# Kernel tuning notes

Hardware: AMD Instinct MI355X
Metric: run time of the kernel (lower is better)

Reference implementation:

```python
import jax, jax.numpy as jnp
import numpy as np

DIM_IN, DIM_H, NUM_CLASSES, TOPK = 384, 512, 2, 6
SCALE = DIM_H ** (-0.5)
LN_EPS = 1e-5


def setup_inputs() -> dict:
    key = jax.random.key(0)
    ks = jax.random.split(key, 16)
    p = lambda k, shape: jax.random.normal(k, shape, dtype=jnp.float32) * 0.02
    return {
        "feats": jax.random.normal(ks[0], (1, 8192, DIM_IN), dtype=jnp.float32),
        "fc1_w": p(ks[1], (DIM_IN, DIM_H)), "fc1_b": jnp.zeros((DIM_H,), jnp.float32),
        "wh_w": p(ks[2], (DIM_H, DIM_H)), "wh_b": jnp.zeros((DIM_H,), jnp.float32),
        "wt_w": p(ks[3], (DIM_H, DIM_H)), "wt_b": jnp.zeros((DIM_H,), jnp.float32),
        "l1_w": p(ks[4], (DIM_H, DIM_H)), "l1_b": jnp.zeros((DIM_H,), jnp.float32),
        "l2_w": p(ks[5], (DIM_H, DIM_H)), "l2_b": jnp.zeros((DIM_H,), jnp.float32),
        "ln_g": jnp.ones((DIM_H,), jnp.float32), "ln_b": jnp.zeros((DIM_H,), jnp.float32),
        "cls_w": p(ks[6], (DIM_H, NUM_CLASSES)), "cls_b": jnp.zeros((NUM_CLASSES,), jnp.float32),
    }


def _wikg_fwd(feats, fc1_w, fc1_b, wh_w, wh_b, wt_w, wt_b,
              l1_w, l1_b, l2_w, l2_b, ln_g, ln_b, cls_w, cls_b):
    lrelu = lambda v: jax.nn.leaky_relu(v, 0.01)
    x = lrelu(feats @ fc1_w + fc1_b)                      # [B,N,D]
    x = (x + x.mean(axis=1, keepdims=True)) * 0.5
    e_h = x @ wh_w + wh_b                                 # [B,N,D]
    e_t = x @ wt_w + wt_b                                 # [B,N,D]
    attn_logit = jnp.einsum('bnd,bmd->bnm', e_h * SCALE, e_t)  # [B,N,N]
    topk_weight, topk_index = jax.lax.top_k(attn_logit, TOPK)  # [B,N,K]
    # gather neighbor tail embeddings: Nb_h[b,n,k] = e_t[b, topk_index[b,n,k]]
    Nb_h = jax.vmap(lambda et, idx: et[idx])(e_t, topk_index)  # [B,N,K,D]
    topk_prob = jax.nn.softmax(topk_weight, axis=2)            # [B,N,K]
    eh_r = topk_prob[..., None] * Nb_h + (1.0 - topk_prob)[..., None] * e_h[:, :, None, :]
    gate = jnp.tanh(e_h[:, :, None, :] + eh_r)                 # [B,N,K,D]
    ka_weight = jnp.einsum('bnkd,bnkd->bnk', Nb_h, gate)       # [B,N,K]
    ka_prob = jax.nn.softmax(ka_weight, axis=2)
    e_Nh = jnp.einsum('bnk,bnkd->bnd', ka_prob, Nb_h)          # [B,N,D]
    # bi-interaction aggregation
    sum_emb = lrelu((e_h + e_Nh) @ l1_w + l1_b)
    bi_emb = lrelu((e_h * e_Nh) @ l2_w + l2_b)
    emb = sum_emb + bi_emb                                     # [B,N,D]
    # dropout is identity in eval mode; mean readout over nodes (B=1 squeezed)
    h = emb[0].mean(axis=0, keepdims=True)                     # [1,D]
    mu = h.mean(axis=-1, keepdims=True)
    var = ((h - mu) ** 2).mean(axis=-1, keepdims=True)
    h = (h - mu) * jax.lax.rsqrt(var + LN_EPS) * ln_g + ln_b
    return h @ cls_w + cls_b                                   # [1,num_classes]


def reference(feats, fc1_w, fc1_b, wh_w, wh_b, wt_w, wt_b,
              l1_w, l1_b, l2_w, l2_b, ln_g, ln_b, cls_w, cls_b):
    return _wikg_fwd(feats, fc1_w, fc1_b, wh_w, wh_b, wt_w, wt_b,
                     l1_w, l1_b, l2_w, l2_b, ln_g, ln_b, cls_w, cls_b)
```

## Files before the change

### kernel.cpp

```cpp
#include <hip/hip_runtime.h>
#include <math.h>

#define DEV __device__ __forceinline__

using frag_ab = __attribute__((ext_vector_type(8))) short;
using frag_cd = __attribute__((ext_vector_type(4))) float;

static constexpr float SCALE_C = 0.04419417382415922f;

DEV unsigned short f2bf(float f) {
    unsigned u = __float_as_uint(f);
    unsigned r = (u + 0x7FFFu + ((u >> 16) & 1u)) >> 16;
    return (unsigned short)r;
}
DEV float bf2f(unsigned short h) { return __uint_as_float(((unsigned)h) << 16); }

DEV void unpack8(uint4 q, float f[8]) {
    f[0] = bf2f((unsigned short)(q.x & 0xFFFFu)); f[1] = bf2f((unsigned short)(q.x >> 16));
    f[2] = bf2f((unsigned short)(q.y & 0xFFFFu)); f[3] = bf2f((unsigned short)(q.y >> 16));
    f[4] = bf2f((unsigned short)(q.z & 0xFFFFu)); f[5] = bf2f((unsigned short)(q.z >> 16));
    f[6] = bf2f((unsigned short)(q.w & 0xFFFFu)); f[7] = bf2f((unsigned short)(q.w >> 16));
}
DEV uint4 pack8(const float f[8]) {
    uint4 q;
    q.x = (unsigned)f2bf(f[0]) | ((unsigned)f2bf(f[1]) << 16);
    q.y = (unsigned)f2bf(f[2]) | ((unsigned)f2bf(f[3]) << 16);
    q.z = (unsigned)f2bf(f[4]) | ((unsigned)f2bf(f[5]) << 16);
    q.w = (unsigned)f2bf(f[6]) | ((unsigned)f2bf(f[7]) << 16);
    return q;
}

DEV unsigned mono(float f) {
    unsigned u = __float_as_uint(f);
    return u ^ ((unsigned)((int)u >> 31) | 0x80000000u);
}
DEV float unmono(unsigned k) {
    unsigned u = (k & 0x80000000u) ? (k & 0x7FFFFFFFu) : ~k;
    return __uint_as_float(u);
}

DEV void gload_lds16(const void* g, void* l) {
    __builtin_amdgcn_global_load_lds(
        (const __attribute__((address_space(1))) void*)g,
        (__attribute__((address_space(3))) void*)l, 16, 0, 0);
}

__global__ void k_conv_bf16(const float* __restrict__ s, unsigned short* __restrict__ d, int n) {
    int i = (blockIdx.x * 256 + threadIdx.x) * 4;
    if (i + 3 < n) {
        float4 v = *(const float4*)(s + i);
        ushort4 o;
        o.x = f2bf(v.x); o.y = f2bf(v.y); o.z = f2bf(v.z); o.w = f2bf(v.w);
        *(ushort4*)(d + i) = o;
    }
}

__global__ void k_transpose_bf16(const float* __restrict__ s, unsigned short* __restrict__ d, int K, int N) {
    int i = blockIdx.x * 256 + threadIdx.x;
    if (i >= K * N) return;
    int n = i / K, k = i - n * K;
    d[i] = f2bf(s[k * N + n]);
}

DEV void stage_async(const unsigned short* __restrict__ g, int ld, int k0, char* lds, int t) {
    const int sub = t >> 3;
    const int b = (t & 7) << 4;
    const int bs = b ^ ((sub & 7) << 4);
    const char* gb = (const char*)(g + k0) + (size_t)sub * (size_t)(ld * 2) + bs;
    char* lb = lds + ((t >> 6) << 10);
    const size_t rstep = (size_t)32 * (ld * 2);
#pragma unroll
    for (int r = 0; r < 4; ++r)
        gload_lds16(gb + r * rstep, lb + r * 4096);
}

DEV void mfma_tile(const char* As, const char* Bs, int lane, int wr, int wc, frag_cd (&acc)[4][4]) {
#pragma unroll
    for (int ks = 0; ks < 2; ++ks) {
        const int boff = ks * 64 + ((lane >> 4) << 4);
        frag_ab av[4];
#pragma unroll
        for (int f = 0; f < 4; ++f) {
            int ra = wr * 64 + f * 16 + (lane & 15);
            av[f] = *(const frag_ab*)(As + ra * 128 + (boff ^ ((ra & 7) << 4)));
        }
#pragma unroll
        for (int j = 0; j < 4; ++j) {
            int rb = wc * 64 + j * 16 + (lane & 15);
            frag_ab bv = *(const frag_ab*)(Bs + rb * 128 + (boff ^ ((rb & 7) << 4)));
#pragma unroll
            for (int i = 0; i < 4; ++i)
                acc[i][j] = __builtin_amdgcn_mfma_f32_16x16x32_bf16(av[i], bv, acc[i][j], 0, 0, 0);
        }
    }
}

template <int ACT, int EPI>
__global__ __launch_bounds__(256, 2) void k_gemm(
    const unsigned short* __restrict__ A0, const unsigned short* __restrict__ A1,
    const unsigned short* __restrict__ B0, const unsigned short* __restrict__ B1,
    const float* __restrict__ bias0, const float* __restrict__ bias1,
    unsigned short* __restrict__ out0, unsigned short* __restrict__ out1,
    float* __restrict__ colsum, int M, int N, int K) {
    __shared__ __align__(16) char smem[65536];
    __shared__ float colacc[128];
    char* sA0 = smem;
    char* sA1 = smem + 16384;
    char* sB0 = smem + 32768;
    char* sB1 = smem + 49152;
    const int z = blockIdx.z;
    const unsigned short* A = z ? A1 : A0;
    const unsigned short* BT = z ? B1 : B0;
    const float* bias = z ? bias1 : bias0;
    unsigned short* out = z ? out1 : out0;
    const int t = threadIdx.x;
    const int lane = t & 63, wid = t >> 6, wr = wid >> 1, wc = wid & 1;
    const int m0 = blockIdx.x * 128, n0 = blockIdx.y * 128;
    if (EPI >= 1 && t < 128) colacc[t] = 0.f;
    const unsigned short* Ap = A + (size_t)m0 * K;
    const unsigned short* Bp = BT + (size_t)n0 * K;
    frag_cd acc[4][4] = {};
    const int nt = K >> 6;
    stage_async(Ap, K, 0, sA0, t);
    stage_async(Bp, K, 0, sB0, t);
    __syncthreads();
#pragma unroll 1
    for (int tt = 0; tt < nt - 2; tt += 2) {
        stage_async(Ap, K, (tt + 1) * 64, sA1, t);
        stage_async(Bp, K, (tt + 1) * 64, sB1, t);
        mfma_tile(sA0, sB0, lane, wr, wc, acc);
        __syncthreads();
        stage_async(Ap, K, (tt + 2) * 64, sA0, t);
        stage_async(Bp, K, (tt + 2) * 64, sB0, t);
        mfma_tile(sA1, sB1, lane, wr, wc, acc);
        __syncthreads();
    }
    stage_async(Ap, K, (nt - 1) * 64, sA1, t);
    stage_async(Bp, K, (nt - 1) * 64, sB1, t);
    mfma_tile(sA0, sB0, lane, wr, wc, acc);
    __syncthreads();
    mfma_tile(sA1, sB1, lane, wr, wc, acc);
    float bval[4];
#pragma unroll
    for (int j = 0; j < 4; ++j) bval[j] = bias[n0 + wc * 64 + j * 16 + (lane & 15)];
#pragma unroll
    for (int i = 0; i < 4; ++i) {
#pragma unroll
        for (int j = 0; j < 4; ++j) {
            float cs = 0.f;
#pragma unroll
            for (int r = 0; r < 4; ++r) {
                float v = acc[i][j][r] + bval[j];
                if (ACT) v = v > 0.f ? v : 0.01f * v;
                if (EPI != 2) {
                    int row = m0 + wr * 64 + i * 16 + (lane >> 4) * 4 + r;
                    int col = n0 + wc * 64 + j * 16 + (lane & 15);
                    out[(size_t)row * N + col] = f2bf(v);
                }
                cs += v;
            }
            if (EPI >= 1) atomicAdd(&colacc[wc * 64 + j * 16 + (lane & 15)], cs);
        }
    }
    if (EPI >= 1) {
        __syncthreads();
        if (t < 128) atomicAdd(&colsum[n0 + t], colacc[t]);
    }
}

__global__ void k_update_x(unsigned short* __restrict__ xb, const float* __restrict__ colsum) {
    int i = (blockIdx.x * 256 + threadIdx.x) * 8;
    uint4 q = *(const uint4*)(xb + i);
    float f[8]; unpack8(q, f);
    int c0 = i & 511;
#pragma unroll
    for (int j = 0; j < 8; ++j) f[j] = 0.5f * (f[j] + colsum[c0 + j] * (1.f / 8192.f));
    *(uint4*)(xb + i) = pack8(f);
}

DEV void kins(unsigned (&v)[6], unsigned k) {
    unsigned m1 = v[0] < k ? v[0] : k;
    unsigned m2 = v[1] < k ? v[1] : k;
    unsigned m3 = v[2] < k ? v[2] : k;
    unsigned m4 = v[3] < k ? v[3] : k;
    unsigned m5 = v[4] < k ? v[4] : k;
    v[0] = v[0] > k ? v[0] : k;
    v[1] = v[1] > m1 ? v[1] : m1;
    v[2] = v[2] > m2 ? v[2] : m2;
    v[3] = v[3] > m3 ? v[3] : m3;
    v[4] = v[4] > m4 ? v[4] : m4;
    v[5] = v[5] > m5 ? v[5] : m5;
}

__global__ __launch_bounds__(256, 2) void k_attn_topk(
    const unsigned short* __restrict__ ehb, const unsigned short* __restrict__ etb,
    unsigned* __restrict__ pk) {
    __shared__ __align__(16) char smem[65536];
    char* sA0 = smem;
    char* sA1 = smem + 16384;
    char* sB0 = smem + 32768;
    char* sB1 = smem + 49152;
    unsigned* Stile = (unsigned*)smem;
    const int t = threadIdx.x;
    const int lane = t & 63, wid = t >> 6, wr = wid >> 1, wc = wid & 1;
    const int m0 = blockIdx.x * 128;
    const int csplit = blockIdx.y;
    const int srow = t >> 1, hh = t & 1;
    const unsigned short* Ap = ehb + (size_t)m0 * 512;
    unsigned ka[6] = {0, 0, 0, 0, 0, 0};
    unsigned kb[6] = {0, 0, 0, 0, 0, 0};

    for (int ct = 0; ct < 4; ++ct) {
        const int n0 = csplit * 512 + ct * 128;
        const unsigned short* Bp = etb + (size_t)n0 * 512;
        frag_cd acc[4][4] = {};
        __syncthreads();
        stage_async(Ap, 512, 0, sA0, t);
        stage_async(Bp, 512, 0, sB0, t);
        __syncthreads();
#pragma unroll 1
        for (int p = 0; p < 3; ++p) {
            stage_async(Ap, 512, (2 * p + 1) * 64, sA1, t);
            stage_async(Bp, 512, (2 * p + 1) * 64, sB1, t);
            mfma_tile(sA0, sB0, lane, wr, wc, acc);
            __syncthreads();
            stage_async(Ap, 512, (2 * p + 2) * 64, sA0, t);
            stage_async(Bp, 512, (2 * p + 2) * 64, sB0, t);
            mfma_tile(sA1, sB1, lane, wr, wc, acc);
            __syncthreads();
        }
        stage_async(Ap, 512, 7 * 64, sA1, t);
        stage_async(Bp, 512, 7 * 64, sB1, t);
        mfma_tile(sA0, sB0, lane, wr, wc, acc);
        __syncthreads();
        mfma_tile(sA1, sB1, lane, wr, wc, acc);
        __syncthreads();
#pragma unroll
        for (int ch = 0; ch < 2; ++ch) {
            if (wc == ch) {
                const unsigned ckb = 8191u - (unsigned)(n0 + ch * 64 + (lane & 15));
#pragma unroll
                for (int i = 0; i < 4; ++i)
#pragma unroll
                    for (int j = 0; j < 4; ++j)
#pragma unroll
                        for (int r = 0; r < 4; ++r) {
                            int row = wr * 64 + i * 16 + (lane >> 4) * 4 + r;
                            int col = j * 16 + (lane & 15);
                            unsigned key = (mono(acc[i][j][r]) & 0xFFFFE000u) | (ckb - j * 16);
                            Stile[row * 68 + col] = key;
                        }
            }
            __syncthreads();
            const uint4* srowp = (const uint4*)(Stile + srow * 68 + hh * 32);
#pragma unroll
            for (int q = 0; q < 8; ++q) {
                uint4 u = srowp[q];
                kins(ka, u.x); kins(kb, u.y);
                kins(ka, u.z); kins(kb, u.w);
            }
            __syncthreads();
        }
    }
#pragma unroll
    for (int j = 0; j < 6; ++j) kins(ka, kb[j]);
#pragma unroll
    for (int j = 0; j < 6; ++j) {
        unsigned ok = (unsigned)__shfl_xor((int)ka[j], 1, 64);
        if (hh == 0) kins(ka, ok);
    }
    if (hh == 0) {
        size_t o = ((size_t)(m0 + srow) * 16 + csplit) * 6;
#pragma unroll
        for (int j = 0; j < 6; ++j) pk[o + j] = ka[j];
    }
}

__global__ void k_merge_topk(const unsigned* __restrict__ pk,
                             float* __restrict__ tw, int* __restrict__ ti) {
    int r = blockIdx.x * 256 + threadIdx.x;
    if (r >= 8192) return;
    unsigned v[6] = {0, 0, 0, 0, 0, 0};
    for (int s2 = 0; s2 < 16; ++s2) {
        const unsigned* p = pk + ((size_t)r * 16 + s2) * 6;
#pragma unroll
        for (int j = 0; j < 6; ++j) kins(v, p[j]);
    }
#pragma unroll
    for (int j = 0; j < 6; ++j) {
        tw[r * 6 + j] = unmono(v[j] & 0xFFFFE000u) * SCALE_C;
        ti[r * 6 + j] = 8191 - (int)(v[j] & 8191u);
    }
}

__global__ __launch_bounds__(256) void k_agg(
    const unsigned short* __restrict__ ehb, const unsigned short* __restrict__ etb,
    const float* __restrict__ tw, const int* __restrict__ ti,
    unsigned short* __restrict__ sb, unsigned short* __restrict__ pb) {
    const int t = threadIdx.x, lane = t & 63, wid = t >> 6;
    const int node = blockIdx.x * 4 + wid;
    const int d0 = lane * 8;
    float w[6]; int idx[6];
#pragma unroll
    for (int k = 0; k < 6; ++k) { w[k] = tw[node * 6 + k]; idx[k] = ti[node * 6 + k]; }
    float mx = w[0];
#pragma unroll
    for (int k = 1; k < 6; ++k) mx = fmaxf(mx, w[k]);
    float pr[6], s = 0.f;
#pragma unroll
    for (int k = 0; k < 6; ++k) { pr[k] = expf(w[k] - mx); s += pr[k]; }
    float inv = 1.f / s;
#pragma unroll
    for (int k = 0; k < 6; ++k) pr[k] *= inv;

    float eh[8]; unpack8(*(const uint4*)(ehb + (size_t)node * 512 + d0), eh);
    float nb[6][8];
#pragma unroll
    for (int k = 0; k < 6; ++k) unpack8(*(const uint4*)(etb + (size_t)idx[k] * 512 + d0), nb[k]);

    float kw[6] = {};
#pragma unroll
    for (int k = 0; k < 6; ++k) {
        float pk2 = pr[k];
#pragma unroll
        for (int j = 0; j < 8; ++j) {
            float ehr = pk2 * nb[k][j] + (1.f - pk2) * eh[j];
            float g = tanhf(eh[j] + ehr);
            kw[k] += nb[k][j] * g;
        }
    }
#pragma unroll
    for (int k = 0; k < 6; ++k)
#pragma unroll
        for (int o = 1; o < 64; o <<= 1) kw[k] += __shfl_xor(kw[k], o, 64);
    float m2 = kw[0];
#pragma unroll
    for (int k = 1; k < 6; ++k) m2 = fmaxf(m2, kw[k]);
    float kp[6], s2 = 0.f;
#pragma unroll
    for (int k = 0; k < 6; ++k) { kp[k] = expf(kw[k] - m2); s2 += kp[k]; }
    float inv2 = 1.f / s2;
#pragma unroll
    for (int k = 0; k < 6; ++k) kp[k] *= inv2;

    float sv[8], pv[8];
#pragma unroll
    for (int j = 0; j < 8; ++j) {
        float en = 0.f;
#pragma unroll
        for (int k = 0; k < 6; ++k) en += kp[k] * nb[k][j];
        sv[j] = eh[j] + en;
        pv[j] = eh[j] * en;
    }
    *(uint4*)(sb + (size_t)node * 512 + d0) = pack8(sv);
    *(uint4*)(pb + (size_t)node * 512 + d0) = pack8(pv);
}

DEV float blocksum512(float v, float* red, int lane, int wid) {
#pragma unroll
    for (int o = 1; o < 64; o <<= 1) v += __shfl_xor(v, o, 64);
    __syncthreads();
    if (lane == 0) red[wid] = v;
    __syncthreads();
    float s = 0.f;
#pragma unroll
    for (int w2 = 0; w2 < 8; ++w2) s += red[w2];
    return s;
}

__global__ __launch_bounds__(512) void k_final(
    const float* __restrict__ colsum_emb, const float* __restrict__ ln_g,
    const float* __restrict__ ln_b, const float* __restrict__ cls_w,
    const float* __restrict__ cls_b, float* __restrict__ out) {
    __shared__ float red[8];
    const int t = threadIdx.x, lane = t & 63, wid = t >> 6;
    float h = colsum_emb[t] * (1.f / 8192.f);
    float mu = blocksum512(h, red, lane, wid) * (1.f / 512.f);
    float d = h - mu;
    float var = blocksum512(d * d, red, lane, wid) * (1.f / 512.f);
    float y = d * rsqrtf(var + 1e-5f) * ln_g[t] + ln_b[t];
    float s0 = blocksum512(y * cls_w[t * 2 + 0], red, lane, wid);
    float s1 = blocksum512(y * cls_w[t * 2 + 1], red, lane, wid);
    if (t == 0) { out[0] = s0 + cls_b[0]; out[1] = s1 + cls_b[1]; }
}

extern "C" void kernel_launch(void* const* d_in, const int* in_sizes, int n_in,
                              void* d_out, int out_size, void* d_ws, size_t ws_size,
                              hipStream_t stream) {
    (void)in_sizes; (void)n_in; (void)out_size; (void)ws_size;
    const float* feats = (const float*)d_in[0];
    const float* fc1_w = (const float*)d_in[1];
    const float* fc1_b = (const float*)d_in[2];
    const float* wh_w  = (const float*)d_in[3];
    const float* wh_b  = (const float*)d_in[4];
    const float* wt_w  = (const float*)d_in[5];
    const float* wt_b  = (const float*)d_in[6];
    const float* l1_w  = (const float*)d_in[7];
    const float* l1_b  = (const float*)d_in[8];
    const float* l2_w  = (const float*)d_in[9];
    const float* l2_b  = (const float*)d_in[10];
    const float* ln_g  = (const float*)d_in[11];
    const float* ln_b  = (const float*)d_in[12];
    const float* cls_w = (const float*)d_in[13];
    const float* cls_b = (const float*)d_in[14];

    char* ws = (char*)d_ws;
    size_t off = 0;
    auto alloc = [&](size_t bytes) {
        char* p = ws + off;
        off += (bytes + 255) & ~(size_t)255;
        return p;
    };
    unsigned short* fb   = (unsigned short*)alloc(8192ull * 384 * 2);
    unsigned short* xb   = (unsigned short*)alloc(8192ull * 512 * 2);
    unsigned short* ehb  = (unsigned short*)alloc(8192ull * 512 * 2);
    unsigned short* etb  = (unsigned short*)alloc(8192ull * 512 * 2);
    unsigned short* sb   = (unsigned short*)alloc(8192ull * 512 * 2);
    unsigned short* pb   = (unsigned short*)alloc(8192ull * 512 * 2);
    unsigned short* wfc1T = (unsigned short*)alloc(512ull * 384 * 2);
    unsigned short* whT  = (unsigned short*)alloc(512ull * 512 * 2);
    unsigned short* wtT  = (unsigned short*)alloc(512ull * 512 * 2);
    unsigned short* l1T  = (unsigned short*)alloc(512ull * 512 * 2);
    unsigned short* l2T  = (unsigned short*)alloc(512ull * 512 * 2);
    float* colsum     = (float*)alloc(512 * 4);
    float* colsum_emb = (float*)alloc(512 * 4);
    unsigned* pk = (unsigned*)alloc(8192ull * 16 * 6 * 4);
    float* tw = (float*)alloc(8192ull * 6 * 4);
    int*   ti = (int*)alloc(8192ull * 6 * 4);

    hipMemsetAsync(colsum, 0, 512 * 4, stream);
    hipMemsetAsync(colsum_emb, 0, 512 * 4, stream);

    k_conv_bf16<<<(8192 * 384 / 4 + 255) / 256, 256, 0, stream>>>(feats, fb, 8192 * 384);
    k_transpose_bf16<<<(512 * 384 + 255) / 256, 256, 0, stream>>>(fc1_w, wfc1T, 384, 512);
    k_transpose_bf16<<<(512 * 512 + 255) / 256, 256, 0, stream>>>(wh_w, whT, 512, 512);
    k_transpose_bf16<<<(512 * 512 + 255) / 256, 256, 0, stream>>>(wt_w, wtT, 512, 512);
    k_transpose_bf16<<<(512 * 512 + 255) / 256, 256, 0, stream>>>(l1_w, l1T, 512, 512);
    k_transpose_bf16<<<(512 * 512 + 255) / 256, 256, 0, stream>>>(l2_w, l2T, 512, 512);

    k_gemm<1, 1><<<dim3(64, 4, 1), 256, 0, stream>>>(
        fb, fb, wfc1T, wfc1T, fc1_b, fc1_b, xb, xb, colsum, 8192, 512, 384);
    k_update_x<<<2048, 256, 0, stream>>>(xb, colsum);
    k_gemm<0, 0><<<dim3(64, 4, 2), 256, 0, stream>>>(
        xb, xb, whT, wtT, wh_b, wt_b, ehb, etb, nullptr, 8192, 512, 512);
    k_attn_topk<<<dim3(64, 16), 256, 0, stream>>>(ehb, etb, pk);
    k_merge_topk<<<32, 256, 0, stream>>>(pk, tw, ti);
    k_agg<<<2048, 256, 0, stream>>>(ehb, etb, tw, ti, sb, pb);
    k_gemm<1, 2><<<dim3(64, 4, 2), 256, 0, stream>>>(
        sb, pb, l1T, l2T, l1_b, l2_b, nullptr, nullptr, colsum_emb, 8192, 512, 512);
    k_final<<<1, 512, 0, stream>>>(colsum_emb, ln_g, ln_b, cls_w, cls_b, (float*)d_out);
}
```

Baseline: 195.6 us.

## Double attention-topk row tile to 256 with 512 threads; fuse prep kernels

The attention/top-k kernel now runs 512-thread blocks that each cover 256 query rows instead of 128. Each staged tail-embedding tile is therefore shared by twice as many rows, which halves global re-reads of e_t. LDS use per block grows to 96KB, so only one block fits per CU. Separately, the feature conversion and the five weight-transpose kernels are merged into one launch, using blockIdx.z to pick the job, to cut launch overhead.

```diff
diff --git a/kernel.cpp b/kernel.cpp
--- a/kernel.cpp
+++ b/kernel.cpp
@@ -45,21 +45,29 @@
         (__attribute__((address_space(3))) void*)l, 16, 0, 0);
 }
 
-__global__ void k_conv_bf16(const float* __restrict__ s, unsigned short* __restrict__ d, int n) {
-    int i = (blockIdx.x * 256 + threadIdx.x) * 4;
-    if (i + 3 < n) {
-        float4 v = *(const float4*)(s + i);
-        ushort4 o;
-        o.x = f2bf(v.x); o.y = f2bf(v.y); o.z = f2bf(v.z); o.w = f2bf(v.w);
-        *(ushort4*)(d + i) = o;
-    }
-}
-
-__global__ void k_transpose_bf16(const float* __restrict__ s, unsigned short* __restrict__ d, int K, int N) {
+__global__ void k_prep(const float* __restrict__ feats, const float* __restrict__ fc1_w,
+                       const float* __restrict__ wh_w, const float* __restrict__ wt_w,
+                       const float* __restrict__ l1_w, const float* __restrict__ l2_w,
+                       unsigned short* __restrict__ fb, unsigned short* __restrict__ wfc1T,
+                       unsigned short* __restrict__ whT, unsigned short* __restrict__ wtT,
+                       unsigned short* __restrict__ l1T, unsigned short* __restrict__ l2T) {
+    const int z = blockIdx.z;
+    if (z == 5) {
+        for (int i = (blockIdx.x * 256 + threadIdx.x) * 4; i < 8192 * 384; i += 1024 * 256 * 4) {
+            float4 v = *(const float4*)(feats + i);
+            ushort4 o;
+            o.x = f2bf(v.x); o.y = f2bf(v.y); o.z = f2bf(v.z); o.w = f2bf(v.w);
+            *(ushort4*)(fb + i) = o;
+        }
+        return;
+    }
+    const float* s = z == 0 ? fc1_w : z == 1 ? wh_w : z == 2 ? wt_w : z == 3 ? l1_w : l2_w;
+    unsigned short* d = z == 0 ? wfc1T : z == 1 ? whT : z == 2 ? wtT : z == 3 ? l1T : l2T;
+    const int K = z == 0 ? 384 : 512;
     int i = blockIdx.x * 256 + threadIdx.x;
-    if (i >= K * N) return;
+    if (i >= K * 512) return;
     int n = i / K, k = i - n * K;
-    d[i] = f2bf(s[k * N + n]);
+    d[i] = f2bf(s[k * 512 + n]);
 }
 
 DEV void stage_async(const unsigned short* __restrict__ g, int ld, int k0, char* lds, int t) {
@@ -72,6 +80,28 @@
 #pragma unroll
     for (int r = 0; r < 4; ++r)
         gload_lds16(gb + r * rstep, lb + r * 4096);
+}
+DEV void stageA512(const unsigned short* __restrict__ g, int ld, int k0, char* lds, int t) {
+    const int sub = t >> 3;
+    const int b = (t & 7) << 4;
+    const int bs = b ^ ((sub & 7) << 4);
+    const char* gb = (const char*)(g + k0) + (size_t)sub * (size_t)(ld * 2) + bs;
+    char* lb = lds + ((t >> 6) << 10);
+    const size_t rstep = (size_t)64 * (ld * 2);
+#pragma unroll
+    for (int r = 0; r < 4; ++r)
+        gload_lds16(gb + r * rstep, lb + r * 8192);
+}
+DEV void stageB512(const unsigned short* __restrict__ g, int ld, int k0, char* lds, int t) {
+    const int sub = t >> 3;
+    const int b = (t & 7) << 4;
+    const int bs = b ^ ((sub & 7) << 4);
+    const char* gb = (const char*)(g + k0) + (size_t)sub * (size_t)(ld * 2) + bs;
+    char* lb = lds + ((t >> 6) << 10);
+    const size_t rstep = (size_t)64 * (ld * 2);
+#pragma unroll
+    for (int r = 0; r < 2; ++r)
+        gload_lds16(gb + r * rstep, lb + r * 8192);
 }
 
 DEV void mfma_tile(const char* As, const char* Bs, int lane, int wr, int wc, frag_cd (&acc)[4][4]) {
@@ -192,18 +222,18 @@
     v[5] = v[5] > m5 ? v[5] : m5;
 }
 
-__global__ __launch_bounds__(256, 2) void k_attn_topk(
+__global__ __launch_bounds__(512, 1) void k_attn_topk(
     const unsigned short* __restrict__ ehb, const unsigned short* __restrict__ etb,
     unsigned* __restrict__ pk) {
-    __shared__ __align__(16) char smem[65536];
+    __shared__ __align__(16) char smem[98304];
     char* sA0 = smem;
-    char* sA1 = smem + 16384;
-    char* sB0 = smem + 32768;
-    char* sB1 = smem + 49152;
+    char* sA1 = smem + 32768;
+    char* sB0 = smem + 65536;
+    char* sB1 = smem + 81920;
     unsigned* Stile = (unsigned*)smem;
     const int t = threadIdx.x;
     const int lane = t & 63, wid = t >> 6, wr = wid >> 1, wc = wid & 1;
-    const int m0 = blockIdx.x * 128;
+    const int m0 = blockIdx.x * 256;
     const int csplit = blockIdx.y;
     const int srow = t >> 1, hh = t & 1;
     const unsigned short* Ap = ehb + (size_t)m0 * 512;
@@ -215,22 +245,22 @@
         const unsigned short* Bp = etb + (size_t)n0 * 512;
         frag_cd acc[4][4] = {};
         __syncthreads();
-        stage_async(Ap, 512, 0, sA0, t);
-        stage_async(Bp, 512, 0, sB0, t);
+        stageA512(Ap, 512, 0, sA0, t);
+        stageB512(Bp, 512, 0, sB0, t);
         __syncthreads();
 #pragma unroll 1
         for (int p = 0; p < 3; ++p) {
-            stage_async(Ap, 512, (2 * p + 1) * 64, sA1, t);
-            stage_async(Bp, 512, (2 * p + 1) * 64, sB1, t);
+            stageA512(Ap, 512, (2 * p + 1) * 64, sA1, t);
+            stageB512(Bp, 512, (2 * p + 1) * 64, sB1, t);
             mfma_tile(sA0, sB0, lane, wr, wc, acc);
             __syncthreads();
-            stage_async(Ap, 512, (2 * p + 2) * 64, sA0, t);
-            stage_async(Bp, 512, (2 * p + 2) * 64, sB0, t);
+            stageA512(Ap, 512, (2 * p + 2) * 64, sA0, t);
+            stageB512(Bp, 512, (2 * p + 2) * 64, sB0, t);
             mfma_tile(sA1, sB1, lane, wr, wc, acc);
             __syncthreads();
         }
-        stage_async(Ap, 512, 7 * 64, sA1, t);
-        stage_async(Bp, 512, 7 * 64, sB1, t);
+        stageA512(Ap, 512, 7 * 64, sA1, t);
+        stageB512(Bp, 512, 7 * 64, sB1, t);
         mfma_tile(sA0, sB0, lane, wr, wc, acc);
         __syncthreads();
         mfma_tile(sA1, sB1, lane, wr, wc, acc);
@@ -431,19 +461,15 @@
     hipMemsetAsync(colsum, 0, 512 * 4, stream);
     hipMemsetAsync(colsum_emb, 0, 512 * 4, stream);
 
-    k_conv_bf16<<<(8192 * 384 / 4 + 255) / 256, 256, 0, stream>>>(feats, fb, 8192 * 384);
-    k_transpose_bf16<<<(512 * 384 + 255) / 256, 256, 0, stream>>>(fc1_w, wfc1T, 384, 512);
-    k_transpose_bf16<<<(512 * 512 + 255) / 256, 256, 0, stream>>>(wh_w, whT, 512, 512);
-    k_transpose_bf16<<<(512 * 512 + 255) / 256, 256, 0, stream>>>(wt_w, wtT, 512, 512);
-    k_transpose_bf16<<<(512 * 512 + 255) / 256, 256, 0, stream>>>(l1_w, l1T, 512, 512);
-    k_transpose_bf16<<<(512 * 512 + 255) / 256, 256, 0, stream>>>(l2_w, l2T, 512, 512);
+    k_prep<<<dim3(1024, 1, 6), 256, 0, stream>>>(
+        feats, fc1_w, wh_w, wt_w, l1_w, l2_w, fb, wfc1T, whT, wtT, l1T, l2T);
 
     k_gemm<1, 1><<<dim3(64, 4, 1), 256, 0, stream>>>(
         fb, fb, wfc1T, wfc1T, fc1_b, fc1_b, xb, xb, colsum, 8192, 512, 384);
     k_update_x<<<2048, 256, 0, stream>>>(xb, colsum);
     k_gemm<0, 0><<<dim3(64, 4, 2), 256, 0, stream>>>(
         xb, xb, whT, wtT, wh_b, wt_b, ehb, etb, nullptr, 8192, 512, 512);
-    k_attn_topk<<<dim3(64, 16), 256, 0, stream>>>(ehb, etb, pk);
+    k_attn_topk<<<dim3(32, 16), 512, 0, stream>>>(ehb, etb, pk);
     k_merge_topk<<<32, 256, 0, stream>>>(pk, tw, ti);
     k_agg<<<2048, 256, 0, stream>>>(ehb, etb, tw, ti, sb, pb);
     k_gemm<1, 2><<<dim3(64, 4, 2), 256, 0, stream>>>(
```

Result: no change. 194.0 us (-0.8%).

## Do top-k selection in registers and fuse weight prep kernels

Applied to the files above, without the earlier changes.

The attention top-k kernel swaps the MFMA operand order so each lane holds one query row's scores across columns. It then keeps a per-row top-6 list in registers and merges lists across lanes with shuffles plus a small LDS exchange between the two column waves, replacing the LDS score-tile write and rescan. It also prefetches the next column tile's first K-slice during the last MFMA step. Separately, the feature conversion and five weight transposes are merged into one launch. The in-register lists add register pressure, which may lower occupancy.

```diff
diff --git a/kernel.cpp b/kernel.cpp
--- a/kernel.cpp
+++ b/kernel.cpp
@@ -45,21 +45,29 @@
         (__attribute__((address_space(3))) void*)l, 16, 0, 0);
 }
 
-__global__ void k_conv_bf16(const float* __restrict__ s, unsigned short* __restrict__ d, int n) {
-    int i = (blockIdx.x * 256 + threadIdx.x) * 4;
-    if (i + 3 < n) {
-        float4 v = *(const float4*)(s + i);
-        ushort4 o;
-        o.x = f2bf(v.x); o.y = f2bf(v.y); o.z = f2bf(v.z); o.w = f2bf(v.w);
-        *(ushort4*)(d + i) = o;
-    }
-}
-
-__global__ void k_transpose_bf16(const float* __restrict__ s, unsigned short* __restrict__ d, int K, int N) {
+__global__ void k_prep(const float* __restrict__ feats, const float* __restrict__ fc1_w,
+                       const float* __restrict__ wh_w, const float* __restrict__ wt_w,
+                       const float* __restrict__ l1_w, const float* __restrict__ l2_w,
+                       unsigned short* __restrict__ fb, unsigned short* __restrict__ wfc1T,
+                       unsigned short* __restrict__ whT, unsigned short* __restrict__ wtT,
+                       unsigned short* __restrict__ l1T, unsigned short* __restrict__ l2T) {
+    const int z = blockIdx.z;
+    if (z == 5) {
+        for (int i = (blockIdx.x * 256 + threadIdx.x) * 4; i < 8192 * 384; i += 1024 * 256 * 4) {
+            float4 v = *(const float4*)(feats + i);
+            ushort4 o;
+            o.x = f2bf(v.x); o.y = f2bf(v.y); o.z = f2bf(v.z); o.w = f2bf(v.w);
+            *(ushort4*)(fb + i) = o;
+        }
+        return;
+    }
+    const float* s = z == 0 ? fc1_w : z == 1 ? wh_w : z == 2 ? wt_w : z == 3 ? l1_w : l2_w;
+    unsigned short* d = z == 0 ? wfc1T : z == 1 ? whT : z == 2 ? wtT : z == 3 ? l1T : l2T;
+    const int K = z == 0 ? 384 : 512;
     int i = blockIdx.x * 256 + threadIdx.x;
-    if (i >= K * N) return;
+    if (i >= K * 512) return;
     int n = i / K, k = i - n * K;
-    d[i] = f2bf(s[k * N + n]);
+    d[i] = f2bf(s[k * 512 + n]);
 }
 
 DEV void stage_async(const unsigned short* __restrict__ g, int ld, int k0, char* lds, int t) {
@@ -91,6 +99,27 @@
 #pragma unroll
             for (int i = 0; i < 4; ++i)
                 acc[i][j] = __builtin_amdgcn_mfma_f32_16x16x32_bf16(av[i], bv, acc[i][j], 0, 0, 0);
+        }
+    }
+}
+
+DEV void mfma_tile_swp(const char* As, const char* Bs, int lane, int wr, int wc, frag_cd (&acc)[4][4]) {
+#pragma unroll
+    for (int ks = 0; ks < 2; ++ks) {
+        const int boff = ks * 64 + ((lane >> 4) << 4);
+        frag_ab av[4];
+#pragma unroll
+        for (int f = 0; f < 4; ++f) {
+            int ra = wr * 64 + f * 16 + (lane & 15);
+            av[f] = *(const frag_ab*)(As + ra * 128 + (boff ^ ((ra & 7) << 4)));
+        }
+#pragma unroll
+        for (int j = 0; j < 4; ++j) {
+            int rb = wc * 64 + j * 16 + (lane & 15);
+            frag_ab bv = *(const frag_ab*)(Bs + rb * 128 + (boff ^ ((rb & 7) << 4)));
+#pragma unroll
+            for (int i = 0; i < 4; ++i)
+                acc[i][j] = __builtin_amdgcn_mfma_f32_16x16x32_bf16(bv, av[i], acc[i][j], 0, 0, 0);
         }
     }
 }
@@ -200,79 +229,88 @@
     char* sA1 = smem + 16384;
     char* sB0 = smem + 32768;
     char* sB1 = smem + 49152;
-    unsigned* Stile = (unsigned*)smem;
+    unsigned* xbuf = (unsigned*)smem;
     const int t = threadIdx.x;
     const int lane = t & 63, wid = t >> 6, wr = wid >> 1, wc = wid & 1;
     const int m0 = blockIdx.x * 128;
     const int csplit = blockIdx.y;
-    const int srow = t >> 1, hh = t & 1;
     const unsigned short* Ap = ehb + (size_t)m0 * 512;
-    unsigned ka[6] = {0, 0, 0, 0, 0, 0};
-    unsigned kb[6] = {0, 0, 0, 0, 0, 0};
-
+    unsigned kl[4][6] = {};
+
+    stage_async(Ap, 512, 0, sA0, t);
+    stage_async(etb + (size_t)(csplit * 512) * 512, 512, 0, sB0, t);
+
+#pragma unroll 1
     for (int ct = 0; ct < 4; ++ct) {
         const int n0 = csplit * 512 + ct * 128;
         const unsigned short* Bp = etb + (size_t)n0 * 512;
         frag_cd acc[4][4] = {};
         __syncthreads();
-        stage_async(Ap, 512, 0, sA0, t);
-        stage_async(Bp, 512, 0, sB0, t);
-        __syncthreads();
 #pragma unroll 1
         for (int p = 0; p < 3; ++p) {
             stage_async(Ap, 512, (2 * p + 1) * 64, sA1, t);
             stage_async(Bp, 512, (2 * p + 1) * 64, sB1, t);
-            mfma_tile(sA0, sB0, lane, wr, wc, acc);
+            mfma_tile_swp(sA0, sB0, lane, wr, wc, acc);
             __syncthreads();
             stage_async(Ap, 512, (2 * p + 2) * 64, sA0, t);
             stage_async(Bp, 512, (2 * p + 2) * 64, sB0, t);
-            mfma_tile(sA1, sB1, lane, wr, wc, acc);
+            mfma_tile_swp(sA1, sB1, lane, wr, wc, acc);
             __syncthreads();
         }
         stage_async(Ap, 512, 7 * 64, sA1, t);
         stage_async(Bp, 512, 7 * 64, sB1, t);
-        mfma_tile(sA0, sB0, lane, wr, wc, acc);
+        mfma_tile_swp(sA0, sB0, lane, wr, wc, acc);
         __syncthreads();
-        mfma_tile(sA1, sB1, lane, wr, wc, acc);
-        __syncthreads();
-#pragma unroll
-        for (int ch = 0; ch < 2; ++ch) {
-            if (wc == ch) {
-                const unsigned ckb = 8191u - (unsigned)(n0 + ch * 64 + (lane & 15));
-#pragma unroll
-                for (int i = 0; i < 4; ++i)
-#pragma unroll
-                    for (int j = 0; j < 4; ++j)
-#pragma unroll
-                        for (int r = 0; r < 4; ++r) {
-                            int row = wr * 64 + i * 16 + (lane >> 4) * 4 + r;
-                            int col = j * 16 + (lane & 15);
-                            unsigned key = (mono(acc[i][j][r]) & 0xFFFFE000u) | (ckb - j * 16);
-                            Stile[row * 68 + col] = key;
-                        }
-            }
-            __syncthreads();
-            const uint4* srowp = (const uint4*)(Stile + srow * 68 + hh * 32);
-#pragma unroll
-            for (int q = 0; q < 8; ++q) {
-                uint4 u = srowp[q];
-                kins(ka, u.x); kins(kb, u.y);
-                kins(ka, u.z); kins(kb, u.w);
-            }
-            __syncthreads();
-        }
-    }
-#pragma unroll
-    for (int j = 0; j < 6; ++j) kins(ka, kb[j]);
-#pragma unroll
-    for (int j = 0; j < 6; ++j) {
-        unsigned ok = (unsigned)__shfl_xor((int)ka[j], 1, 64);
-        if (hh == 0) kins(ka, ok);
-    }
-    if (hh == 0) {
-        size_t o = ((size_t)(m0 + srow) * 16 + csplit) * 6;
-#pragma unroll
-        for (int j = 0; j < 6; ++j) pk[o + j] = ka[j];
+        if (ct < 3) {
+            stage_async(Ap, 512, 0, sA0, t);
+            stage_async(etb + (size_t)(n0 + 128) * 512, 512, 0, sB0, t);
+        }
+        mfma_tile_swp(sA1, sB1, lane, wr, wc, acc);
+        const int base_ck = 8191 - (n0 + wc * 64 + ((lane >> 4) << 2));
+#pragma unroll
+        for (int i = 0; i < 4; ++i)
+#pragma unroll
+            for (int j = 0; j < 4; ++j)
+#pragma unroll
+                for (int r = 0; r < 4; ++r) {
+                    unsigned key = (mono(acc[i][j][r]) & 0xFFFFE000u) |
+                                   (unsigned)(base_ck - j * 16 - r);
+                    kins(kl[i], key);
+                }
+    }
+#pragma unroll
+    for (int i = 0; i < 4; ++i) {
+#pragma unroll
+        for (int j = 0; j < 6; ++j) {
+            unsigned ok = (unsigned)__shfl_xor((int)kl[i][j], 16, 64);
+            kins(kl[i], ok);
+        }
+#pragma unroll
+        for (int j = 0; j < 6; ++j) {
+            unsigned ok = (unsigned)__shfl_xor((int)kl[i][j], 32, 64);
+            kins(kl[i], ok);
+        }
+    }
+    __syncthreads();
+    if (wc == 1 && (lane >> 4) == 0) {
+#pragma unroll
+        for (int i = 0; i < 4; ++i) {
+            int row = wr * 64 + i * 16 + lane;
+#pragma unroll
+            for (int j = 0; j < 6; ++j) xbuf[row * 6 + j] = kl[i][j];
+        }
+    }
+    __syncthreads();
+    if (wc == 0 && (lane >> 4) == 0) {
+#pragma unroll
+        for (int i = 0; i < 4; ++i) {
+            int row = wr * 64 + i * 16 + lane;
+#pragma unroll
+            for (int j = 0; j < 6; ++j) kins(kl[i], xbuf[row * 6 + j]);
+            size_t o = ((size_t)(m0 + row) * 16 + csplit) * 6;
+#pragma unroll
+            for (int j = 0; j < 6; ++j) pk[o + j] = kl[i][j];
+        }
     }
 }
 
@@ -431,12 +469,8 @@
     hipMemsetAsync(colsum, 0, 512 * 4, stream);
     hipMemsetAsync(colsum_emb, 0, 512 * 4, stream);
 
-    k_conv_bf16<<<(8192 * 384 / 4 + 255) / 256, 256, 0, stream>>>(feats, fb, 8192 * 384);
-    k_transpose_bf16<<<(512 * 384 + 255) / 256, 256, 0, stream>>>(fc1_w, wfc1T, 384, 512);
-    k_transpose_bf16<<<(512 * 512 + 255) / 256, 256, 0, stream>>>(wh_w, whT, 512, 512);
-    k_transpose_bf16<<<(512 * 512 + 255) / 256, 256, 0, stream>>>(wt_w, wtT, 512, 512);
-    k_transpose_bf16<<<(512 * 512 + 255) / 256, 256, 0, stream>>>(l1_w, l1T, 512, 512);
-    k_transpose_bf16<<<(512 * 512 + 255) / 256, 256, 0, stream>>>(l2_w, l2T, 512, 512);
+    k_prep<<<dim3(1024, 1, 6), 256, 0, stream>>>(
+        feats, fc1_w, wh_w, wt_w, l1_w, l2_w, fb, wfc1T, whT, wtT, l1T, l2T);
 
     k_gemm<1, 1><<<dim3(64, 4, 1), 256, 0, stream>>>(
         fb, fb, wfc1T, wfc1T, fc1_b, fc1_b, xb, xb, colsum, 8192, 512, 384);
```

Result: faster. 182.7 us (-6.6%).
